# Kernel optimization log

Measured on AMD Instinct MI355X. Metric: run time of the kernel, lower is better.

## Reference

```python
import jax, jax.numpy as jnp
import numpy as np

N = 100000      # number of edge features (rows of feats)
M = 800000      # number of triplets
HID = 128
HEADS = 8
DH = HID // HEADS


def setup_inputs() -> dict:
    key = jax.random.key(0)
    ks = jax.random.split(key, 10)
    s = 1.0 / np.sqrt(HID)
    inp = {
        "feats": jax.random.normal(ks[0], (N, HID), dtype=jnp.float32),
        "idx_kj": jax.random.randint(ks[1], (M,), 0, N, dtype=jnp.int64),
        "idx_ji": jax.random.randint(ks[2], (M,), 0, N, dtype=jnp.int64),
        "Wv": jax.random.uniform(ks[3], (HID, HID), jnp.float32, -s, s),
        "Wq": jax.random.uniform(ks[4], (HID, HID), jnp.float32, -s, s),
        "Wk": jax.random.uniform(ks[5], (HID, HID), jnp.float32, -s, s),
        "W1": jax.random.uniform(ks[6], (HID, HID), jnp.float32, -s, s),
        "b1": jax.random.uniform(ks[7], (HID,), jnp.float32, -s, s),
        "W2": jax.random.uniform(ks[8], (HID, HID), jnp.float32, -s, s),
        "b2": jax.random.uniform(ks[9], (HID,), jnp.float32, -s, s),
    }
    return inp


def reference(feats, idx_kj, idx_ji, Wv, Wq, Wk, W1, b1, W2, b2):
    # Projections (no bias), reshape to [N, H, Dh]
    v = (feats @ Wv.T).reshape(N, HEADS, DH)
    k = (feats @ Wk.T).reshape(N, HEADS, DH)
    q = (feats @ Wq.T).reshape(N, HEADS, DH)

    # edge-indexed attention scores: [M, H, 1]
    att = jnp.sum(q[idx_kj] * k[idx_ji], axis=-1, keepdims=True)
    att = jnp.exp(jax.nn.leaky_relu(att, negative_slope=0.2))  # unsafe softmax, as in source

    # segment-sum normalizer over destination index idx_ji: [N, H, 1]
    denom = jax.ops.segment_sum(att, idx_ji, num_segments=N)
    att = att / denom[idx_ji]

    # weighted V gather-scatter: [M, HID] -> [N, HID]
    v_att = (v[idx_kj] * att).reshape(M, HID)
    agg = jax.ops.segment_sum(v_att, idx_ji, num_segments=N)  # v_clone after +scatter-v

    v_flat = v.reshape(N, HID)
    # ResidualLayer (dropout in eval mode -> identity): v + relu(lin2(relu(lin1(agg))))
    h = jax.nn.relu(agg @ W1.T + b1)
    h = jax.nn.relu(h @ W2.T + b2)
    return v_flat + h
```

## Files before the change

### kernel.cpp

```cpp
#include <hip/hip_runtime.h>
#include <hip/hip_bf16.h>
#include <math.h>

#define N_NODES 100000
#define M_EDGES 800000
#define HID 128
#define HEADS 8
#define DH 16
#define SCAN_NB ((N_NODES + 1023) / 1024)

typedef __attribute__((ext_vector_type(8))) short short8;
typedef __attribute__((ext_vector_type(4))) float floatx4;

__device__ __forceinline__ ushort f32_to_bf16(float x) {
    __hip_bfloat16 h = __float2bfloat16(x);
    union { __hip_bfloat16 h; ushort u; } c; c.h = h;
    return c.u;
}
__device__ __forceinline__ float bf16_bits_to_f32(ushort u) {
    union { unsigned int i; float f; } c; c.i = ((unsigned int)u) << 16;
    return c.f;
}
__device__ __forceinline__ float bf16pair_lo(unsigned int p) {
    union { unsigned int i; float f; } c; c.i = p << 16; return c.f;
}
__device__ __forceinline__ float bf16pair_hi(unsigned int p) {
    union { unsigned int i; float f; } c; c.i = p & 0xffff0000u; return c.f;
}

__global__ __launch_bounds__(256) void cvt_w_kernel(
    const float* __restrict__ Wq, const float* __restrict__ Wk, const float* __restrict__ Wv,
    const float* __restrict__ W1, const float* __restrict__ W2,
    ushort* __restrict__ dq, ushort* __restrict__ dk, ushort* __restrict__ dv,
    ushort* __restrict__ d1, ushort* __restrict__ d2)
{
    int i = blockIdx.x * 256 + threadIdx.x;
    int w = i >> 14;
    int o = i & 16383;
    int j    = o & 7;
    int lane = (o >> 3) & 63;
    int f    = o >> 9;
    int t    = f & 7, ks = f >> 3;
    int row  = t * 16 + (lane & 15);
    int col  = ks * 32 + (lane >> 4) * 8 + j;
    const float* s[5] = {Wq, Wk, Wv, W1, W2};
    ushort*      d[5] = {dq, dk, dv, d1, d2};
    d[w][o] = f32_to_bf16(s[w][row * HID + col]);
}

__global__ __launch_bounds__(256) void qkv_mfma_kernel(
    const float* __restrict__ feats,
    const ushort* __restrict__ Wq16, const ushort* __restrict__ Wk16, const ushort* __restrict__ Wv16,
    ushort* __restrict__ qv16, ushort* __restrict__ k16)
{
    const int tid  = threadIdx.x;
    const int wave = tid >> 6;
    const int lane = tid & 63;
    const int row0 = blockIdx.x * 128 + wave * 32;
    const int lrow = lane & 15;
    const int lk   = (lane >> 4) * 8;
    const int crow = (lane >> 4) * 4;

    short8 afrag[2][4];
    bool tvalid[2];
    #pragma unroll
    for (int r = 0; r < 2; ++r) {
        int rr = row0 + r * 16;
        tvalid[r] = (rr < N_NODES);
        const float* arow = feats + (size_t)((tvalid[r] ? rr : 0) + lrow) * HID + lk;
        #pragma unroll
        for (int ks = 0; ks < 4; ++ks) {
            float4 f0 = *(const float4*)(arow + ks * 32);
            float4 f1 = *(const float4*)(arow + ks * 32 + 4);
            short8 a;
            a[0] = (short)f32_to_bf16(f0.x); a[1] = (short)f32_to_bf16(f0.y);
            a[2] = (short)f32_to_bf16(f0.z); a[3] = (short)f32_to_bf16(f0.w);
            a[4] = (short)f32_to_bf16(f1.x); a[5] = (short)f32_to_bf16(f1.y);
            a[6] = (short)f32_to_bf16(f1.z); a[7] = (short)f32_to_bf16(f1.w);
            afrag[r][ks] = a;
        }
    }

    const ushort* Ws[3] = {Wq16, Wk16, Wv16};
    ushort* Ob[3]; int Ostride[3];
    Ob[0] = qv16;       Ostride[0] = 256;
    Ob[1] = k16;        Ostride[1] = 128;
    Ob[2] = qv16 + 128; Ostride[2] = 256;

    #pragma unroll
    for (int w = 0; w < 3; ++w) {
        const ushort* Wf = Ws[w];

        floatx4 acc[2][8];
        #pragma unroll
        for (int r = 0; r < 2; ++r)
            #pragma unroll
            for (int t = 0; t < 8; ++t) acc[r][t] = (floatx4)(0.f);

        #pragma unroll
        for (int ks = 0; ks < 4; ++ks) {
            short8 B[8];
            #pragma unroll
            for (int t = 0; t < 8; ++t)
                B[t] = *(const short8*)&Wf[(ks * 8 + t) * 512 + lane * 8];
            #pragma unroll
            for (int t = 0; t < 8; ++t) {
                acc[0][t] = __builtin_amdgcn_mfma_f32_16x16x32_bf16(B[t], afrag[0][ks], acc[0][t], 0, 0, 0);
                acc[1][t] = __builtin_amdgcn_mfma_f32_16x16x32_bf16(B[t], afrag[1][ks], acc[1][t], 0, 0, 0);
            }
        }

        #pragma unroll
        for (int r = 0; r < 2; ++r) {
            if (tvalid[r]) {
                ushort* O = Ob[w] + (size_t)(row0 + r * 16 + lrow) * Ostride[w];
                #pragma unroll
                for (int t = 0; t < 8; ++t) {
                    ushort4 o;
                    o.x = f32_to_bf16(acc[r][t][0]); o.y = f32_to_bf16(acc[r][t][1]);
                    o.z = f32_to_bf16(acc[r][t][2]); o.w = f32_to_bf16(acc[r][t][3]);
                    *(ushort4*)(O + t * 16 + crow) = o;
                }
            }
        }
    }
}

__global__ __launch_bounds__(256) void hist_kernel(
    const int* __restrict__ idx_ji, int* __restrict__ count)
{
    int m = blockIdx.x * 256 + threadIdx.x;
    if (m < M_EDGES) atomicAdd(&count[idx_ji[m]], 1);
}

__global__ __launch_bounds__(256) void scan_blocksum_kernel(
    const int* __restrict__ count, int* __restrict__ blocksum)
{
    __shared__ int s[256];
    const int tid = threadIdx.x;
    const int base = blockIdx.x * 1024 + tid * 4;
    int sum = 0;
    if (base + 3 < N_NODES) {
        int4 c = *(const int4*)(count + base);
        sum = c.x + c.y + c.z + c.w;
    } else {
        #pragma unroll
        for (int j = 0; j < 4; ++j) if (base + j < N_NODES) sum += count[base + j];
    }
    s[tid] = sum;
    __syncthreads();
    for (int off = 128; off > 0; off >>= 1) {
        if (tid < off) s[tid] += s[tid + off];
        __syncthreads();
    }
    if (tid == 0) blocksum[blockIdx.x] = s[0];
}

__global__ __launch_bounds__(128) void scan_top_kernel(int* __restrict__ blocksum)
{
    __shared__ int s[128];
    const int t = threadIdx.x;
    int v = (t < SCAN_NB) ? blocksum[t] : 0;
    s[t] = v;
    __syncthreads();
    for (int off = 1; off < 128; off <<= 1) {
        int x = (t >= off) ? s[t - off] : 0;
        __syncthreads();
        s[t] += x;
        __syncthreads();
    }
    if (t < SCAN_NB) blocksum[t] = s[t] - v;
}

__global__ __launch_bounds__(256) void scan_write_kernel(
    const int* __restrict__ count, const int* __restrict__ blocksum,
    int* __restrict__ offsets, int* __restrict__ cursor)
{
    __shared__ int s[256];
    const int tid = threadIdx.x;
    const int base = blockIdx.x * 1024 + tid * 4;
    int c0 = 0, c1 = 0, c2 = 0, c3 = 0;
    if (base + 3 < N_NODES) {
        int4 c = *(const int4*)(count + base);
        c0 = c.x; c1 = c.y; c2 = c.z; c3 = c.w;
    } else {
        if (base     < N_NODES) c0 = count[base];
        if (base + 1 < N_NODES) c1 = count[base + 1];
        if (base + 2 < N_NODES) c2 = count[base + 2];
        if (base + 3 < N_NODES) c3 = count[base + 3];
    }
    const int tsum = c0 + c1 + c2 + c3;
    s[tid] = tsum;
    __syncthreads();
    for (int off = 1; off < 256; off <<= 1) {
        int x = (tid >= off) ? s[tid - off] : 0;
        __syncthreads();
        s[tid] += x;
        __syncthreads();
    }
    int o0 = s[tid] - tsum + blocksum[blockIdx.x];
    int o1 = o0 + c0, o2 = o1 + c1, o3 = o2 + c2;
    if (base + 3 < N_NODES) {
        *(int4*)(offsets + base) = make_int4(o0, o1, o2, o3);
        *(int4*)(cursor  + base) = make_int4(o0, o1, o2, o3);
    } else {
        if (base     < N_NODES) { offsets[base]     = o0; cursor[base]     = o0; }
        if (base + 1 < N_NODES) { offsets[base + 1] = o1; cursor[base + 1] = o1; }
        if (base + 2 < N_NODES) { offsets[base + 2] = o2; cursor[base + 2] = o2; }
        if (base + 3 < N_NODES) { offsets[base + 3] = o3; cursor[base + 3] = o3; }
    }
}

__global__ __launch_bounds__(256) void fill_kernel(
    const int* __restrict__ idx_ji, const int* __restrict__ idx_kj,
    int* __restrict__ cursor, int* __restrict__ edge_kj)
{
    int m = blockIdx.x * 256 + threadIdx.x;
    if (m < M_EDGES) {
        int pos = atomicAdd(&cursor[idx_ji[m]], 1);
        edge_kj[pos] = idx_kj[m];
    }
}

__device__ __forceinline__ float dot8(const uint4& qp, const float* kn) {
    const unsigned int* q = (const unsigned int*)&qp;
    float p = 0.f;
    #pragma unroll
    for (int j = 0; j < 4; ++j)
        p += bf16pair_lo(q[j]) * kn[2*j] + bf16pair_hi(q[j]) * kn[2*j+1];
    return p;
}
__device__ __forceinline__ void axpy8(float* acc, float s, const uint4& vp) {
    const unsigned int* v = (const unsigned int*)&vp;
    #pragma unroll
    for (int j = 0; j < 4; ++j) {
        acc[2*j]   += s * bf16pair_lo(v[j]);
        acc[2*j+1] += s * bf16pair_hi(v[j]);
    }
}

__global__ __launch_bounds__(256) void aggregate_kernel(
    const int* __restrict__ edge_kj, const int* __restrict__ offsets,
    const int* __restrict__ count, const ushort* __restrict__ qv16,
    const ushort* __restrict__ k16, ushort* __restrict__ agg16)
{
    const int gid  = blockIdx.x * 256 + threadIdx.x;
    const int node = gid >> 4;
    const int l16  = threadIdx.x & 15;
    if (node >= N_NODES) return;

    const int deg  = count[node];
    const int base = offsets[node];

    float kn[8];
    {
        uint4 kp = *(const uint4*)(k16 + (size_t)node * HID + l16 * 8);
        const unsigned int* kw = (const unsigned int*)&kp;
        #pragma unroll
        for (int j = 0; j < 4; ++j) {
            kn[2*j]   = bf16pair_lo(kw[j]);
            kn[2*j+1] = bf16pair_hi(kw[j]);
        }
    }

    float acc[8] = {0.f,0.f,0.f,0.f,0.f,0.f,0.f,0.f};
    float d = 0.f;

    const ushort* qvb = qv16 + l16 * 8;

    int e = 0;
    for (; e + 4 <= deg; e += 4) {
        const int kj0 = edge_kj[base + e + 0];
        const int kj1 = edge_kj[base + e + 1];
        const int kj2 = edge_kj[base + e + 2];
        const int kj3 = edge_kj[base + e + 3];
        const ushort* r0 = qvb + (size_t)kj0 * 256;
        const ushort* r1 = qvb + (size_t)kj1 * 256;
        const ushort* r2 = qvb + (size_t)kj2 * 256;
        const ushort* r3 = qvb + (size_t)kj3 * 256;
        uint4 qp0 = *(const uint4*)r0;  uint4 vp0 = *(const uint4*)(r0 + 128);
        uint4 qp1 = *(const uint4*)r1;  uint4 vp1 = *(const uint4*)(r1 + 128);
        uint4 qp2 = *(const uint4*)r2;  uint4 vp2 = *(const uint4*)(r2 + 128);
        uint4 qp3 = *(const uint4*)r3;  uint4 vp3 = *(const uint4*)(r3 + 128);

        float p0 = dot8(qp0, kn);
        float p1 = dot8(qp1, kn);
        float p2 = dot8(qp2, kn);
        float p3 = dot8(qp3, kn);
        p0 += __shfl_xor(p0, 1);
        p1 += __shfl_xor(p1, 1);
        p2 += __shfl_xor(p2, 1);
        p3 += __shfl_xor(p3, 1);
        float s0 = __expf(fmaxf(p0, 0.2f * p0));
        float s1 = __expf(fmaxf(p1, 0.2f * p1));
        float s2 = __expf(fmaxf(p2, 0.2f * p2));
        float s3 = __expf(fmaxf(p3, 0.2f * p3));
        d += (s0 + s1) + (s2 + s3);
        axpy8(acc, s0, vp0);
        axpy8(acc, s1, vp1);
        axpy8(acc, s2, vp2);
        axpy8(acc, s3, vp3);
    }
    if (e + 2 <= deg) {
        const int kj0 = edge_kj[base + e];
        const int kj1 = edge_kj[base + e + 1];
        const ushort* r0 = qvb + (size_t)kj0 * 256;
        const ushort* r1 = qvb + (size_t)kj1 * 256;
        uint4 qp0 = *(const uint4*)r0;  uint4 vp0 = *(const uint4*)(r0 + 128);
        uint4 qp1 = *(const uint4*)r1;  uint4 vp1 = *(const uint4*)(r1 + 128);
        float p0 = dot8(qp0, kn);
        float p1 = dot8(qp1, kn);
        p0 += __shfl_xor(p0, 1);
        p1 += __shfl_xor(p1, 1);
        float s0 = __expf(fmaxf(p0, 0.2f * p0));
        float s1 = __expf(fmaxf(p1, 0.2f * p1));
        d += s0 + s1;
        axpy8(acc, s0, vp0);
        axpy8(acc, s1, vp1);
        e += 2;
    }
    if (e < deg) {
        const int kj0 = edge_kj[base + e];
        const ushort* r0 = qvb + (size_t)kj0 * 256;
        uint4 qp0 = *(const uint4*)r0;  uint4 vp0 = *(const uint4*)(r0 + 128);
        float p0 = dot8(qp0, kn);
        p0 += __shfl_xor(p0, 1);
        float s0 = __expf(fmaxf(p0, 0.2f * p0));
        d += s0;
        axpy8(acc, s0, vp0);
    }

    const float inv = (deg > 0) ? 1.f / d : 0.f;
    uint4 o;
    unsigned int* ow = (unsigned int*)&o;
    #pragma unroll
    for (int j = 0; j < 4; ++j)
        ow[j] = (unsigned int)f32_to_bf16(acc[2*j] * inv)
              | ((unsigned int)f32_to_bf16(acc[2*j+1] * inv) << 16);
    *(uint4*)(agg16 + (size_t)node * HID + l16 * 8) = o;
}

__global__ __launch_bounds__(256) void mlp_mfma_kernel(
    const ushort* __restrict__ agg16, const ushort* __restrict__ qv16,
    const ushort* __restrict__ W1_16, const float* __restrict__ b1,
    const ushort* __restrict__ W2_16, const float* __restrict__ b2,
    float* __restrict__ out)
{
    __shared__ ushort h1s[16384];
    const int tid  = threadIdx.x;
    const int wave = tid >> 6;
    const int lane = tid & 63;
    const int row0 = blockIdx.x * 128 + wave * 32;
    const int lrow = lane & 15;
    const int lk   = (lane >> 4) * 8;
    const int crow = (lane >> 4) * 4;

    short8 afrag[2][4];
    bool tvalid[2];
    #pragma unroll
    for (int r = 0; r < 2; ++r) {
        int rr = row0 + r * 16;
        tvalid[r] = (rr < N_NODES);
        const ushort* arow = agg16 + (size_t)((tvalid[r] ? rr : 0) + lrow) * HID + lk;
        #pragma unroll
        for (int ks = 0; ks < 4; ++ks)
            afrag[r][ks] = *(const short8*)(arow + ks * 32);
    }

    {
        floatx4 acc[2][8];
        #pragma unroll
        for (int r = 0; r < 2; ++r)
            #pragma unroll
            for (int t = 0; t < 8; ++t) acc[r][t] = (floatx4)(0.f);
        #pragma unroll
        for (int ks = 0; ks < 4; ++ks) {
            short8 B[8];
            #pragma unroll
            for (int t = 0; t < 8; ++t)
                B[t] = *(const short8*)&W1_16[(ks * 8 + t) * 512 + lane * 8];
            #pragma unroll
            for (int t = 0; t < 8; ++t) {
                acc[0][t] = __builtin_amdgcn_mfma_f32_16x16x32_bf16(B[t], afrag[0][ks], acc[0][t], 0, 0, 0);
                acc[1][t] = __builtin_amdgcn_mfma_f32_16x16x32_bf16(B[t], afrag[1][ks], acc[1][t], 0, 0, 0);
            }
        }
        #pragma unroll
        for (int r = 0; r < 2; ++r) {
            ushort* tile = &h1s[(wave * 2 + r) * 2048];
            #pragma unroll
            for (int t = 0; t < 8; ++t) {
                float4 bias = *(const float4*)(b1 + t * 16 + crow);
                ushort4 o;
                o.x = f32_to_bf16(fmaxf(acc[r][t][0] + bias.x, 0.f));
                o.y = f32_to_bf16(fmaxf(acc[r][t][1] + bias.y, 0.f));
                o.z = f32_to_bf16(fmaxf(acc[r][t][2] + bias.z, 0.f));
                o.w = f32_to_bf16(fmaxf(acc[r][t][3] + bias.w, 0.f));
                int ks   = t >> 1;
                int quad = (t & 1) * 2 + (crow >> 3);
                int j0   = crow & 4;
                *(ushort4*)(tile + (ks * 64 + quad * 16 + lrow) * 8 + j0) = o;
            }
        }
    }
    __syncthreads();

    {
        short8 hfrag[2][4];
        #pragma unroll
        for (int r = 0; r < 2; ++r) {
            const ushort* tile = &h1s[(wave * 2 + r) * 2048];
            #pragma unroll
            for (int ks = 0; ks < 4; ++ks)
                hfrag[r][ks] = *(const short8*)(tile + (ks * 64 + lane) * 8);
        }
        floatx4 acc[2][8];
        #pragma unroll
        for (int r = 0; r < 2; ++r)
            #pragma unroll
            for (int t = 0; t < 8; ++t) acc[r][t] = (floatx4)(0.f);
        #pragma unroll
        for (int ks = 0; ks < 4; ++ks) {
            short8 B[8];
            #pragma unroll
            for (int t = 0; t < 8; ++t)
                B[t] = *(const short8*)&W2_16[(ks * 8 + t) * 512 + lane * 8];
            #pragma unroll
            for (int t = 0; t < 8; ++t) {
                acc[0][t] = __builtin_amdgcn_mfma_f32_16x16x32_bf16(B[t], hfrag[0][ks], acc[0][t], 0, 0, 0);
                acc[1][t] = __builtin_amdgcn_mfma_f32_16x16x32_bf16(B[t], hfrag[1][ks], acc[1][t], 0, 0, 0);
            }
        }
        #pragma unroll
        for (int r = 0; r < 2; ++r) {
            if (tvalid[r]) {
                const size_t nrow = (size_t)(row0 + r * 16 + lrow);
                const ushort* vrow = qv16 + nrow * 256 + 128;
                float* orow = out + nrow * HID;
                #pragma unroll
                for (int t = 0; t < 8; ++t) {
                    float4 bias = *(const float4*)(b2 + t * 16 + crow);
                    ushort4 vv = *(const ushort4*)(vrow + t * 16 + crow);
                    float4 o;
                    o.x = bf16_bits_to_f32(vv.x) + fmaxf(acc[r][t][0] + bias.x, 0.f);
                    o.y = bf16_bits_to_f32(vv.y) + fmaxf(acc[r][t][1] + bias.y, 0.f);
                    o.z = bf16_bits_to_f32(vv.z) + fmaxf(acc[r][t][2] + bias.z, 0.f);
                    o.w = bf16_bits_to_f32(vv.w) + fmaxf(acc[r][t][3] + bias.w, 0.f);
                    *(float4*)(orow + t * 16 + crow) = o;
                }
            }
        }
    }
}

extern "C" void kernel_launch(void* const* d_in, const int* in_sizes, int n_in,
                              void* d_out, int out_size, void* d_ws, size_t ws_size,
                              hipStream_t stream) {
    const float* feats  = (const float*)d_in[0];
    const int*   idx_kj = (const int*)d_in[1];
    const int*   idx_ji = (const int*)d_in[2];
    const float* Wv     = (const float*)d_in[3];
    const float* Wq     = (const float*)d_in[4];
    const float* Wk     = (const float*)d_in[5];
    const float* W1     = (const float*)d_in[6];
    const float* b1     = (const float*)d_in[7];
    const float* W2     = (const float*)d_in[8];
    const float* b2     = (const float*)d_in[9];
    float* out = (float*)d_out;

    ushort* qv16    = (ushort*)d_ws;
    ushort* k16     = qv16    + (size_t)N_NODES * 256;
    ushort* agg16   = k16     + (size_t)N_NODES * HID;
    ushort* Wq16    = agg16   + (size_t)N_NODES * HID;
    ushort* Wk16    = Wq16 + HID * HID;
    ushort* Wv16    = Wk16 + HID * HID;
    ushort* W116    = Wv16 + HID * HID;
    ushort* W216    = W116 + HID * HID;
    int* count      = (int*)(W216 + HID * HID);
    int* offsets    = count + N_NODES;
    int* cursor     = offsets + N_NODES;
    int* blocksum   = cursor + N_NODES;
    int* edge_kj    = blocksum + ((SCAN_NB + 3) & ~3);

    hipMemsetAsync(count, 0, N_NODES * sizeof(int), stream);

    cvt_w_kernel<<<(5 * HID * HID + 255) / 256, 256, 0, stream>>>(
        Wq, Wk, Wv, W1, W2, Wq16, Wk16, Wv16, W116, W216);

    qkv_mfma_kernel<<<(N_NODES + 127) / 128, 256, 0, stream>>>(
        feats, Wq16, Wk16, Wv16, qv16, k16);

    hist_kernel<<<(M_EDGES + 255) / 256, 256, 0, stream>>>(idx_ji, count);
    scan_blocksum_kernel<<<SCAN_NB, 256, 0, stream>>>(count, blocksum);
    scan_top_kernel<<<1, 128, 0, stream>>>(blocksum);
    scan_write_kernel<<<SCAN_NB, 256, 0, stream>>>(count, blocksum, offsets, cursor);
    fill_kernel<<<(M_EDGES + 255) / 256, 256, 0, stream>>>(idx_ji, idx_kj, cursor, edge_kj);

    aggregate_kernel<<<((size_t)N_NODES * 16 + 255) / 256, 256, 0, stream>>>(
        edge_kj, offsets, count, qv16, k16, agg16);

    mlp_mfma_kernel<<<(N_NODES + 127) / 128, 256, 0, stream>>>(
        agg16, qv16, W116, b1, W216, b2, out);
}
```

Measured before the change: 335.0 us.

## Fuse weight conversion into GEMM kernels via LDS staging and fold histogram into QKV

Removes the separate weight-conversion kernel: each QKV and MLP block now reads fp32 weights, converts them to bf16 in the MFMA fragment layout and stages them in shared memory before the matmuls. The edge histogram atomics are also moved into the tail of the QKV kernel as a grid-stride loop, removing another launch. This saves two kernel launches and reads B fragments from LDS instead of global memory. In exchange, every block redoes the weight conversion (782 blocks × 3 or 2 weights), adds barriers and 32KB or more of LDS per block, which may lower occupancy.

```diff
diff --git a/kernel.cpp b/kernel.cpp
--- a/kernel.cpp
+++ b/kernel.cpp
@@ -28,31 +28,37 @@
     union { unsigned int i; float f; } c; c.i = p & 0xffff0000u; return c.f;
 }
 
-__global__ __launch_bounds__(256) void cvt_w_kernel(
-    const float* __restrict__ Wq, const float* __restrict__ Wk, const float* __restrict__ Wv,
-    const float* __restrict__ W1, const float* __restrict__ W2,
-    ushort* __restrict__ dq, ushort* __restrict__ dk, ushort* __restrict__ dv,
-    ushort* __restrict__ d1, ushort* __restrict__ d2)
-{
-    int i = blockIdx.x * 256 + threadIdx.x;
-    int w = i >> 14;
-    int o = i & 16383;
-    int j    = o & 7;
-    int lane = (o >> 3) & 63;
-    int f    = o >> 9;
-    int t    = f & 7, ks = f >> 3;
-    int row  = t * 16 + (lane & 15);
-    int col  = ks * 32 + (lane >> 4) * 8 + j;
-    const float* s[5] = {Wq, Wk, Wv, W1, W2};
-    ushort*      d[5] = {dq, dk, dv, d1, d2};
-    d[w][o] = f32_to_bf16(s[w][row * HID + col]);
+__device__ __forceinline__ void stage_w_cvt(const float* __restrict__ W,
+                                            ushort* __restrict__ lds, int tid)
+{
+    #pragma unroll
+    for (int i = 0; i < 8; ++i) {
+        int idx  = i * 256 + tid;
+        int f    = idx >> 6;
+        int lane = idx & 63;
+        int t    = f & 7, ks = f >> 3;
+        int row  = t * 16 + (lane & 15);
+        int col  = ks * 32 + (lane >> 4) * 8;
+        const float* src = W + row * HID + col;
+        float4 f0 = *(const float4*)(src);
+        float4 f1 = *(const float4*)(src + 4);
+        ushort4 o0, o1;
+        o0.x = f32_to_bf16(f0.x); o0.y = f32_to_bf16(f0.y);
+        o0.z = f32_to_bf16(f0.z); o0.w = f32_to_bf16(f0.w);
+        o1.x = f32_to_bf16(f1.x); o1.y = f32_to_bf16(f1.y);
+        o1.z = f32_to_bf16(f1.z); o1.w = f32_to_bf16(f1.w);
+        *(ushort4*)(lds + idx * 8)     = o0;
+        *(ushort4*)(lds + idx * 8 + 4) = o1;
+    }
 }
 
 __global__ __launch_bounds__(256) void qkv_mfma_kernel(
     const float* __restrict__ feats,
-    const ushort* __restrict__ Wq16, const ushort* __restrict__ Wk16, const ushort* __restrict__ Wv16,
-    ushort* __restrict__ qv16, ushort* __restrict__ k16)
-{
+    const float* __restrict__ Wq, const float* __restrict__ Wk, const float* __restrict__ Wv,
+    ushort* __restrict__ qv16, ushort* __restrict__ k16,
+    const int* __restrict__ idx_ji, int* __restrict__ count)
+{
+    __shared__ ushort wlds[16384];
     const int tid  = threadIdx.x;
     const int wave = tid >> 6;
     const int lane = tid & 63;
@@ -81,7 +87,7 @@
         }
     }
 
-    const ushort* Ws[3] = {Wq16, Wk16, Wv16};
+    const float* Ws[3] = {Wq, Wk, Wv};
     ushort* Ob[3]; int Ostride[3];
     Ob[0] = qv16;       Ostride[0] = 256;
     Ob[1] = k16;        Ostride[1] = 128;
@@ -89,7 +95,9 @@
 
     #pragma unroll
     for (int w = 0; w < 3; ++w) {
-        const ushort* Wf = Ws[w];
+        __syncthreads();
+        stage_w_cvt(Ws[w], wlds, tid);
+        __syncthreads();
 
         floatx4 acc[2][8];
         #pragma unroll
@@ -102,7 +110,7 @@
             short8 B[8];
             #pragma unroll
             for (int t = 0; t < 8; ++t)
-                B[t] = *(const short8*)&Wf[(ks * 8 + t) * 512 + lane * 8];
+                B[t] = *(const short8*)&wlds[(ks * 8 + t) * 512 + lane * 8];
             #pragma unroll
             for (int t = 0; t < 8; ++t) {
                 acc[0][t] = __builtin_amdgcn_mfma_f32_16x16x32_bf16(B[t], afrag[0][ks], acc[0][t], 0, 0, 0);
@@ -124,13 +132,10 @@
             }
         }
     }
-}
-
-__global__ __launch_bounds__(256) void hist_kernel(
-    const int* __restrict__ idx_ji, int* __restrict__ count)
-{
-    int m = blockIdx.x * 256 + threadIdx.x;
-    if (m < M_EDGES) atomicAdd(&count[idx_ji[m]], 1);
+
+    const int gstride = gridDim.x * 256;
+    for (int m = blockIdx.x * 256 + tid; m < M_EDGES; m += gstride)
+        atomicAdd(&count[idx_ji[m]], 1);
 }
 
 __global__ __launch_bounds__(256) void scan_blocksum_kernel(
@@ -342,10 +347,11 @@
 
 __global__ __launch_bounds__(256) void mlp_mfma_kernel(
     const ushort* __restrict__ agg16, const ushort* __restrict__ qv16,
-    const ushort* __restrict__ W1_16, const float* __restrict__ b1,
-    const ushort* __restrict__ W2_16, const float* __restrict__ b2,
+    const float* __restrict__ W1, const float* __restrict__ b1,
+    const float* __restrict__ W2, const float* __restrict__ b2,
     float* __restrict__ out)
 {
+    __shared__ ushort wlds[16384];
     __shared__ ushort h1s[16384];
     const int tid  = threadIdx.x;
     const int wave = tid >> 6;
@@ -367,6 +373,9 @@
             afrag[r][ks] = *(const short8*)(arow + ks * 32);
     }
 
+    stage_w_cvt(W1, wlds, tid);
+    __syncthreads();
+
     {
         floatx4 acc[2][8];
         #pragma unroll
@@ -378,7 +387,7 @@
             short8 B[8];
             #pragma unroll
             for (int t = 0; t < 8; ++t)
-                B[t] = *(const short8*)&W1_16[(ks * 8 + t) * 512 + lane * 8];
+                B[t] = *(const short8*)&wlds[(ks * 8 + t) * 512 + lane * 8];
             #pragma unroll
             for (int t = 0; t < 8; ++t) {
                 acc[0][t] = __builtin_amdgcn_mfma_f32_16x16x32_bf16(B[t], afrag[0][ks], acc[0][t], 0, 0, 0);
@@ -404,6 +413,8 @@
         }
     }
     __syncthreads();
+    stage_w_cvt(W2, wlds, tid);
+    __syncthreads();
 
     {
         short8 hfrag[2][4];
@@ -424,7 +435,7 @@
             short8 B[8];
             #pragma unroll
             for (int t = 0; t < 8; ++t)
-                B[t] = *(const short8*)&W2_16[(ks * 8 + t) * 512 + lane * 8];
+                B[t] = *(const short8*)&wlds[(ks * 8 + t) * 512 + lane * 8];
             #pragma unroll
             for (int t = 0; t < 8; ++t) {
                 acc[0][t] = __builtin_amdgcn_mfma_f32_16x16x32_bf16(B[t], hfrag[0][ks], acc[0][t], 0, 0, 0);
@@ -471,12 +482,7 @@
     ushort* qv16    = (ushort*)d_ws;
     ushort* k16     = qv16    + (size_t)N_NODES * 256;
     ushort* agg16   = k16     + (size_t)N_NODES * HID;
-    ushort* Wq16    = agg16   + (size_t)N_NODES * HID;
-    ushort* Wk16    = Wq16 + HID * HID;
-    ushort* Wv16    = Wk16 + HID * HID;
-    ushort* W116    = Wv16 + HID * HID;
-    ushort* W216    = W116 + HID * HID;
-    int* count      = (int*)(W216 + HID * HID);
+    int* count      = (int*)(agg16 + (size_t)N_NODES * HID);
     int* offsets    = count + N_NODES;
     int* cursor     = offsets + N_NODES;
     int* blocksum   = cursor + N_NODES;
@@ -484,13 +490,9 @@
 
     hipMemsetAsync(count, 0, N_NODES * sizeof(int), stream);
 
-    cvt_w_kernel<<<(5 * HID * HID + 255) / 256, 256, 0, stream>>>(
-        Wq, Wk, Wv, W1, W2, Wq16, Wk16, Wv16, W116, W216);
-
     qkv_mfma_kernel<<<(N_NODES + 127) / 128, 256, 0, stream>>>(
-        feats, Wq16, Wk16, Wv16, qv16, k16);
-
-    hist_kernel<<<(M_EDGES + 255) / 256, 256, 0, stream>>>(idx_ji, count);
+        feats, Wq, Wk, Wv, qv16, k16, idx_ji, count);
+
     scan_blocksum_kernel<<<SCAN_NB, 256, 0, stream>>>(count, blocksum);
     scan_top_kernel<<<1, 128, 0, stream>>>(blocksum);
     scan_write_kernel<<<SCAN_NB, 256, 0, stream>>>(count, blocksum, offsets, cursor);
@@ -500,5 +502,5 @@
         edge_kj, offsets, count, qv16, k16, agg16);
 
     mlp_mfma_kernel<<<(N_NODES + 127) / 128, 256, 0, stream>>>(
-        agg16, qv16, W116, b1, W216, b2, out);
-}
+        agg16, qv16, W1, b1, W2, b2, out);
+}
```

Measured after the change: 335.5 us. About the same (+0.2%).

## Fold memset and scan-top into kernels, stage weights in LDS for GEMMs

Applied to the files above, without the earlier changes.

Zeroing of the count array moves into the weight-conversion kernel, so the separate memset goes away. The single-block scan_top kernel is removed, and each scan_write block now reduces the preceding block sums itself. Both changes cut launch count and serialization. The QKV and MLP GEMMs copy each bf16 weight matrix into LDS once per block instead of every wave reading it from global/L2, and the MLP now stages the hidden activations through a small padded per-wave LDS scratch. The cost is extra __syncthreads and 32KB+ of LDS per block, which may reduce occupancy.

```diff
diff --git a/kernel.cpp b/kernel.cpp
--- a/kernel.cpp
+++ b/kernel.cpp
@@ -32,20 +32,34 @@
     const float* __restrict__ Wq, const float* __restrict__ Wk, const float* __restrict__ Wv,
     const float* __restrict__ W1, const float* __restrict__ W2,
     ushort* __restrict__ dq, ushort* __restrict__ dk, ushort* __restrict__ dv,
-    ushort* __restrict__ d1, ushort* __restrict__ d2)
+    ushort* __restrict__ d1, ushort* __restrict__ d2,
+    int* __restrict__ count)
 {
     int i = blockIdx.x * 256 + threadIdx.x;
-    int w = i >> 14;
-    int o = i & 16383;
-    int j    = o & 7;
-    int lane = (o >> 3) & 63;
-    int f    = o >> 9;
-    int t    = f & 7, ks = f >> 3;
-    int row  = t * 16 + (lane & 15);
-    int col  = ks * 32 + (lane >> 4) * 8 + j;
-    const float* s[5] = {Wq, Wk, Wv, W1, W2};
-    ushort*      d[5] = {dq, dk, dv, d1, d2};
-    d[w][o] = f32_to_bf16(s[w][row * HID + col]);
+    if (i < 5 * 16384) {
+        int w = i >> 14;
+        int o = i & 16383;
+        int j    = o & 7;
+        int lane = (o >> 3) & 63;
+        int f    = o >> 9;
+        int t    = f & 7, ks = f >> 3;
+        int row  = t * 16 + (lane & 15);
+        int col  = ks * 32 + (lane >> 4) * 8 + j;
+        const float* s[5] = {Wq, Wk, Wv, W1, W2};
+        ushort*      d[5] = {dq, dk, dv, d1, d2};
+        d[w][o] = f32_to_bf16(s[w][row * HID + col]);
+    }
+    if (i < N_NODES) count[i] = 0;
+}
+
+__device__ __forceinline__ void stage_w_lin(const ushort* __restrict__ Wf,
+                                            ushort* __restrict__ lds, int tid)
+{
+    #pragma unroll
+    for (int i = 0; i < 8; ++i) {
+        int idx = (i * 256 + tid) * 8;
+        *(uint4*)(lds + idx) = *(const uint4*)(Wf + idx);
+    }
 }
 
 __global__ __launch_bounds__(256) void qkv_mfma_kernel(
@@ -53,6 +67,7 @@
     const ushort* __restrict__ Wq16, const ushort* __restrict__ Wk16, const ushort* __restrict__ Wv16,
     ushort* __restrict__ qv16, ushort* __restrict__ k16)
 {
+    __shared__ ushort wlds[16384];
     const int tid  = threadIdx.x;
     const int wave = tid >> 6;
     const int lane = tid & 63;
@@ -89,7 +104,9 @@
 
     #pragma unroll
     for (int w = 0; w < 3; ++w) {
-        const ushort* Wf = Ws[w];
+        __syncthreads();
+        stage_w_lin(Ws[w], wlds, tid);
+        __syncthreads();
 
         floatx4 acc[2][8];
         #pragma unroll
@@ -102,7 +119,7 @@
             short8 B[8];
             #pragma unroll
             for (int t = 0; t < 8; ++t)
-                B[t] = *(const short8*)&Wf[(ks * 8 + t) * 512 + lane * 8];
+                B[t] = *(const short8*)&wlds[(ks * 8 + t) * 512 + lane * 8];
             #pragma unroll
             for (int t = 0; t < 8; ++t) {
                 acc[0][t] = __builtin_amdgcn_mfma_f32_16x16x32_bf16(B[t], afrag[0][ks], acc[0][t], 0, 0, 0);
@@ -156,29 +173,23 @@
     if (tid == 0) blocksum[blockIdx.x] = s[0];
 }
 
-__global__ __launch_bounds__(128) void scan_top_kernel(int* __restrict__ blocksum)
-{
-    __shared__ int s[128];
-    const int t = threadIdx.x;
-    int v = (t < SCAN_NB) ? blocksum[t] : 0;
-    s[t] = v;
-    __syncthreads();
-    for (int off = 1; off < 128; off <<= 1) {
-        int x = (t >= off) ? s[t - off] : 0;
-        __syncthreads();
-        s[t] += x;
-        __syncthreads();
-    }
-    if (t < SCAN_NB) blocksum[t] = s[t] - v;
-}
-
 __global__ __launch_bounds__(256) void scan_write_kernel(
     const int* __restrict__ count, const int* __restrict__ blocksum,
     int* __restrict__ offsets, int* __restrict__ cursor)
 {
     __shared__ int s[256];
+    __shared__ int sb[256];
     const int tid = threadIdx.x;
     const int base = blockIdx.x * 1024 + tid * 4;
+
+    sb[tid] = (tid < (int)blockIdx.x && tid < SCAN_NB) ? blocksum[tid] : 0;
+    __syncthreads();
+    for (int off = 128; off > 0; off >>= 1) {
+        if (tid < off) sb[tid] += sb[tid + off];
+        __syncthreads();
+    }
+    const int bbase = sb[0];
+
     int c0 = 0, c1 = 0, c2 = 0, c3 = 0;
     if (base + 3 < N_NODES) {
         int4 c = *(const int4*)(count + base);
@@ -198,7 +209,7 @@
         s[tid] += x;
         __syncthreads();
     }
-    int o0 = s[tid] - tsum + blocksum[blockIdx.x];
+    int o0 = s[tid] - tsum + bbase;
     int o1 = o0 + c0, o2 = o1 + c1, o3 = o2 + c2;
     if (base + 3 < N_NODES) {
         *(int4*)(offsets + base) = make_int4(o0, o1, o2, o3);
@@ -342,11 +353,12 @@
 
 __global__ __launch_bounds__(256) void mlp_mfma_kernel(
     const ushort* __restrict__ agg16, const ushort* __restrict__ qv16,
-    const ushort* __restrict__ W1_16, const float* __restrict__ b1,
-    const ushort* __restrict__ W2_16, const float* __restrict__ b2,
+    const ushort* __restrict__ W1f, const float* __restrict__ b1,
+    const ushort* __restrict__ W2f, const float* __restrict__ b2,
     float* __restrict__ out)
 {
-    __shared__ ushort h1s[16384];
+    __shared__ ushort wlds[16384];
+    __shared__ ushort hs[4][16 * 136];
     const int tid  = threadIdx.x;
     const int wave = tid >> 6;
     const int lane = tid & 63;
@@ -367,6 +379,44 @@
             afrag[r][ks] = *(const short8*)(arow + ks * 32);
     }
 
+    stage_w_lin(W1f, wlds, tid);
+    __syncthreads();
+
+    short8 hfrag[2][4];
+    ushort* sc = &hs[wave][0];
+    #pragma unroll
+    for (int r = 0; r < 2; ++r) {
+        floatx4 acc[8];
+        #pragma unroll
+        for (int t = 0; t < 8; ++t) acc[t] = (floatx4)(0.f);
+        #pragma unroll
+        for (int ks = 0; ks < 4; ++ks) {
+            short8 B[8];
+            #pragma unroll
+            for (int t = 0; t < 8; ++t)
+                B[t] = *(const short8*)&wlds[(ks * 8 + t) * 512 + lane * 8];
+            #pragma unroll
+            for (int t = 0; t < 8; ++t)
+                acc[t] = __builtin_amdgcn_mfma_f32_16x16x32_bf16(B[t], afrag[r][ks], acc[t], 0, 0, 0);
+        }
+        #pragma unroll
+        for (int t = 0; t < 8; ++t) {
+            float4 bias = *(const float4*)(b1 + t * 16 + crow);
+            ushort4 o;
+            o.x = f32_to_bf16(fmaxf(acc[t][0] + bias.x, 0.f));
+            o.y = f32_to_bf16(fmaxf(acc[t][1] + bias.y, 0.f));
+            o.z = f32_to_bf16(fmaxf(acc[t][2] + bias.z, 0.f));
+            o.w = f32_to_bf16(fmaxf(acc[t][3] + bias.w, 0.f));
+            *(ushort4*)(sc + lrow * 136 + t * 16 + crow) = o;
+        }
+        #pragma unroll
+        for (int ks = 0; ks < 4; ++ks)
+            hfrag[r][ks] = *(const short8*)(sc + lrow * 136 + ks * 32 + lk);
+    }
+    __syncthreads();
+    stage_w_lin(W2f, wlds, tid);
+    __syncthreads();
+
     {
         floatx4 acc[2][8];
         #pragma unroll
@@ -378,53 +428,7 @@
             short8 B[8];
             #pragma unroll
             for (int t = 0; t < 8; ++t)
-                B[t] = *(const short8*)&W1_16[(ks * 8 + t) * 512 + lane * 8];
-            #pragma unroll
-            for (int t = 0; t < 8; ++t) {
-                acc[0][t] = __builtin_amdgcn_mfma_f32_16x16x32_bf16(B[t], afrag[0][ks], acc[0][t], 0, 0, 0);
-                acc[1][t] = __builtin_amdgcn_mfma_f32_16x16x32_bf16(B[t], afrag[1][ks], acc[1][t], 0, 0, 0);
-            }
-        }
-        #pragma unroll
-        for (int r = 0; r < 2; ++r) {
-            ushort* tile = &h1s[(wave * 2 + r) * 2048];
-            #pragma unroll
-            for (int t = 0; t < 8; ++t) {
-                float4 bias = *(const float4*)(b1 + t * 16 + crow);
-                ushort4 o;
-                o.x = f32_to_bf16(fmaxf(acc[r][t][0] + bias.x, 0.f));
-                o.y = f32_to_bf16(fmaxf(acc[r][t][1] + bias.y, 0.f));
-                o.z = f32_to_bf16(fmaxf(acc[r][t][2] + bias.z, 0.f));
-                o.w = f32_to_bf16(fmaxf(acc[r][t][3] + bias.w, 0.f));
-                int ks   = t >> 1;
-                int quad = (t & 1) * 2 + (crow >> 3);
-                int j0   = crow & 4;
-                *(ushort4*)(tile + (ks * 64 + quad * 16 + lrow) * 8 + j0) = o;
-            }
-        }
-    }
-    __syncthreads();
-
-    {
-        short8 hfrag[2][4];
-        #pragma unroll
-        for (int r = 0; r < 2; ++r) {
-            const ushort* tile = &h1s[(wave * 2 + r) * 2048];
-            #pragma unroll
-            for (int ks = 0; ks < 4; ++ks)
-                hfrag[r][ks] = *(const short8*)(tile + (ks * 64 + lane) * 8);
-        }
-        floatx4 acc[2][8];
-        #pragma unroll
-        for (int r = 0; r < 2; ++r)
-            #pragma unroll
-            for (int t = 0; t < 8; ++t) acc[r][t] = (floatx4)(0.f);
-        #pragma unroll
-        for (int ks = 0; ks < 4; ++ks) {
-            short8 B[8];
-            #pragma unroll
-            for (int t = 0; t < 8; ++t)
-                B[t] = *(const short8*)&W2_16[(ks * 8 + t) * 512 + lane * 8];
+                B[t] = *(const short8*)&wlds[(ks * 8 + t) * 512 + lane * 8];
             #pragma unroll
             for (int t = 0; t < 8; ++t) {
                 acc[0][t] = __builtin_amdgcn_mfma_f32_16x16x32_bf16(B[t], hfrag[0][ks], acc[0][t], 0, 0, 0);
@@ -482,17 +486,14 @@
     int* blocksum   = cursor + N_NODES;
     int* edge_kj    = blocksum + ((SCAN_NB + 3) & ~3);
 
-    hipMemsetAsync(count, 0, N_NODES * sizeof(int), stream);
-
-    cvt_w_kernel<<<(5 * HID * HID + 255) / 256, 256, 0, stream>>>(
-        Wq, Wk, Wv, W1, W2, Wq16, Wk16, Wv16, W116, W216);
+    cvt_w_kernel<<<(N_NODES + 255) / 256, 256, 0, stream>>>(
+        Wq, Wk, Wv, W1, W2, Wq16, Wk16, Wv16, W116, W216, count);
 
     qkv_mfma_kernel<<<(N_NODES + 127) / 128, 256, 0, stream>>>(
         feats, Wq16, Wk16, Wv16, qv16, k16);
 
     hist_kernel<<<(M_EDGES + 255) / 256, 256, 0, stream>>>(idx_ji, count);
     scan_blocksum_kernel<<<SCAN_NB, 256, 0, stream>>>(count, blocksum);
-    scan_top_kernel<<<1, 128, 0, stream>>>(blocksum);
     scan_write_kernel<<<SCAN_NB, 256, 0, stream>>>(count, blocksum, offsets, cursor);
     fill_kernel<<<(M_EDGES + 255) / 256, 256, 0, stream>>>(idx_ji, idx_kj, cursor, edge_kj);
 
```

Measured after the change: 322.8 us. -3.6%, faster.
